# Performance work log

Hardware: AMD Instinct MI355X
Metric: run time of the kernel (lower is better)

Reference implementation:

```python
import jax, jax.numpy as jnp
import numpy as np

N, DIN, DOUT = 8192, 512, 256


def setup_inputs() -> dict:
    key = jax.random.key(0)
    ks = jax.random.split(key, 8)
    s_in = 1.0 / np.sqrt(DIN)   # ~ torch Linear default init scale
    s_out = 1.0 / np.sqrt(DOUT)
    return {
        "x": jax.random.normal(ks[0], (N, DIN), jnp.float32),
        "Wm": jax.random.normal(ks[1], (DIN, DOUT), jnp.float32) * s_in,
        "Wn": jax.random.normal(ks[2], (DIN, DOUT), jnp.float32) * s_in,
        "Wr": jax.random.normal(ks[3], (DIN, DOUT), jnp.float32) * s_in,
        "Wt": jax.random.normal(ks[4], (DIN, DOUT), jnp.float32) * s_in,
        "Wrg": jax.random.normal(ks[5], (DOUT, DOUT), jnp.float32) * s_out,
        "brg": jnp.zeros((DOUT,), jnp.float32),
        "Wlg": jax.random.normal(ks[6], (DOUT, DOUT), jnp.float32) * s_out,
        "blg": jnp.zeros((DOUT,), jnp.float32),
        "Wp": jax.random.normal(ks[7], (DOUT, 1), jnp.float32) * s_out,
        "bp": jnp.zeros((1,), jnp.float32),
    }


def reference(x, Wm, Wn, Wr, Wt, Wrg, brg, Wlg, blg, Wp, bp):
    n = x.shape[0]
    xm = x @ Wm                      # [N, 256]
    xn = x @ Wn                      # [N, 256]
    # pairwise Euclidean distance via GEMM trick (avoids O(N^2*D) diff tensor)
    sq = (jnp.sum(xm * xm, axis=-1)[:, None]
          + jnp.sum(xn * xn, axis=-1)[None, :]
          - 2.0 * (xm @ xn.T))       # [N, N]
    dist = jnp.sqrt(jnp.maximum(sq, 0.0)) * 0.5
    exps = jnp.exp(-dist) / (n / 64.0)
    eye = jnp.eye(n, dtype=x.dtype)
    adj = exps * (1.0 - eye) + eye   # unit diagonal, scaled off-diagonal
    xr = adj @ (x @ Wr)              # graph conv: [N,N]@[N,256]
    xl = x @ Wt
    w = jax.nn.sigmoid(xr @ Wrg + brg + xl @ Wlg + blg)
    feat = (1.0 - w) * xr + w * xl   # gated fusion
    score = feat @ Wp + bp           # [N, 1]
    return adj, score
```

## Files before the change

### kernel.cpp

```cpp
#include <hip/hip_runtime.h>
#include <stdint.h>

typedef __attribute__((ext_vector_type(8))) short bf16x8;
typedef __attribute__((ext_vector_type(4))) float f32x4;

__device__ __forceinline__ unsigned short f2bf(float f){
  unsigned u = __float_as_uint(f);
  u += 0x7FFFu + ((u >> 16) & 1u);
  return (unsigned short)(u >> 16);
}
__device__ __forceinline__ float bf2f(unsigned short s){
  return __uint_as_float(((unsigned)s) << 16);
}

__device__ __forceinline__ int lds_off(int r, int b){
  return r * 128 + (b ^ ((r & 7) << 4));
}

__device__ __forceinline__ void cp16(const unsigned short* g, unsigned short* l){
  __builtin_amdgcn_global_load_lds(
      (const __attribute__((address_space(1))) unsigned int*)g,
      (__attribute__((address_space(3))) unsigned int*)l, 16, 0, 0);
}

template<int ROWS, int NT>
__device__ __forceinline__ void stage_async(unsigned short* lds, const unsigned short* g,
                                            long row0, long stride, long k0, int tid){
#pragma unroll
  for (int c = tid; c < ROWS * 8; c += NT){
    int r = c >> 3, s = c & 7;
    int ss = s ^ (r & 7);
    cp16(g + (row0 + r) * stride + k0 + ss * 8, lds + (long)(c & ~63) * 8);
  }
}

template<int NT>
__device__ __forceinline__ void stage_adj(unsigned short* lds, const float* adj,
                                          long row0, long j, int tid){
#pragma unroll
  for (int u = 0; u < 1024 / NT; ++u){
    int c = tid + u * NT;
    int rr = c >> 3, s = c & 7;
    const f32x4* src = (const f32x4*)(adj + (row0 + rr) * 8192 + j + s * 8);
    f32x4 v0 = __builtin_nontemporal_load(src);
    f32x4 v1 = __builtin_nontemporal_load(src + 1);
    unsigned short tb[8] = { f2bf(v0[0]), f2bf(v0[1]), f2bf(v0[2]), f2bf(v0[3]),
                             f2bf(v1[0]), f2bf(v1[1]), f2bf(v1[2]), f2bf(v1[3]) };
    *(uint4*)((char*)lds + lds_off(rr, s * 16)) = *(const uint4*)tb;
  }
}

__device__ __forceinline__ int xcd_swz(int bid, int nwg){
  int q = nwg >> 3;
  return (bid & 7) * q + (bid >> 3);
}

__global__ __launch_bounds__(256) void k_prep(const float* x, const float* Wm, const float* Wn,
    const float* Wr, const float* Wt, const float* Wrg, const float* Wlg, const float* bp,
    unsigned short* WT, unsigned short* WcatT, unsigned short* xbf, float* nm, float* nn,
    float* score){
  long id = (long)blockIdx.x * 256 + threadIdx.x;
  if (id < 1024L * 512){
    int n = (int)(id >> 9), k = (int)(id & 511);
    const float* W = (n < 256) ? Wm : ((n < 512) ? Wn : ((n < 768) ? Wr : Wt));
    WT[id] = f2bf(W[(long)k * 256 + (n & 255)]);
  }
  if (id < 256L * 512){
    int n = (int)(id >> 9), k = (int)(id & 511);
    WcatT[id] = f2bf(k < 256 ? Wrg[(long)k * 256 + n] : Wlg[(long)(k - 256) * 256 + n]);
  }
  if (id < 8192){ score[id] = bp[0]; nm[id] = 0.f; nn[id] = 0.f; }
  long xe = id * 8;
  float4 v0 = *(const float4*)(x + xe);
  float4 v1 = *(const float4*)(x + xe + 4);
  unsigned short t[8] = { f2bf(v0.x), f2bf(v0.y), f2bf(v0.z), f2bf(v0.w),
                          f2bf(v1.x), f2bf(v1.y), f2bf(v1.z), f2bf(v1.w) };
  *(uint4*)(xbf + xe) = *(const uint4*)t;
}

__global__ __launch_bounds__(256, 3) void k_gemmA(const unsigned short* xbf, const unsigned short* WT,
    unsigned short* xm, unsigned short* xn, unsigned short* xwrT, unsigned short* xl,
    float* nm, float* nn){
  __shared__ unsigned short ldsA[128 * 64];
  __shared__ unsigned short ldsB[128 * 64];
  int tid = threadIdx.x, lane = tid & 63, w = tid >> 6;
  int r = lane & 15, gq = lane >> 4;
  int wi = w >> 1, wc = w & 1;
  int swz = xcd_swz(blockIdx.x, 512);
  int bm = swz & 63, bn = swz >> 6;

  f32x4 acc[4][4];
  f32x4 zero = {0.f, 0.f, 0.f, 0.f};
#pragma unroll
  for (int m = 0; m < 4; ++m)
#pragma unroll
    for (int n = 0; n < 4; ++n) acc[m][n] = zero;

  for (int k0 = 0; k0 < 512; k0 += 64){
    __syncthreads();
    stage_async<128, 256>(ldsA, xbf, (long)bm * 128, 512, k0, tid);
    stage_async<128, 256>(ldsB, WT, (long)bn * 128, 512, k0, tid);
    __syncthreads();
#pragma unroll
    for (int ks = 0; ks < 2; ++ks){
      int bb = ks * 64 + gq * 16;
      bf16x8 a[4], b[4];
#pragma unroll
      for (int m = 0; m < 4; ++m)
        a[m] = *(const bf16x8*)((const char*)ldsA + lds_off(wi * 64 + m * 16 + r, bb));
#pragma unroll
      for (int n = 0; n < 4; ++n)
        b[n] = *(const bf16x8*)((const char*)ldsB + lds_off(wc * 64 + n * 16 + r, bb));
#pragma unroll
      for (int m = 0; m < 4; ++m)
#pragma unroll
        for (int n = 0; n < 4; ++n)
          acc[m][n] = __builtin_amdgcn_mfma_f32_16x16x32_bf16(b[n], a[m], acc[m][n], 0, 0, 0);
    }
  }
#pragma unroll
  for (int m = 0; m < 4; ++m){
    int i = bm * 128 + wi * 64 + m * 16 + r;
#pragma unroll
    for (int n = 0; n < 4; ++n){
      int ng = bn * 128 + wc * 64 + n * 16 + gq * 4;
      int sector = ng >> 8, nc = ng & 255;
      unsigned short p[4] = { f2bf(acc[m][n][0]), f2bf(acc[m][n][1]),
                              f2bf(acc[m][n][2]), f2bf(acc[m][n][3]) };
      if (sector == 2){
#pragma unroll
        for (int q = 0; q < 4; ++q) xwrT[(long)(nc + q) * 8192 + i] = p[q];
      } else {
        unsigned short* dst = sector == 0 ? xm : (sector == 1 ? xn : xl);
        *(uint2*)(dst + (long)i * 256 + nc) = *(const uint2*)p;
      }
    }
    if (bn < 4){
      float s = 0.f;
#pragma unroll
      for (int n = 0; n < 4; ++n)
#pragma unroll
        for (int q = 0; q < 4; ++q) s += acc[m][n][q] * acc[m][n][q];
      s += __shfl_xor(s, 16);
      s += __shfl_xor(s, 32);
      if (gq == 0) atomicAdd(((bn < 2) ? nm : nn) + i, s);
    }
  }
}

__global__ __launch_bounds__(256, 2) void k_adj(const unsigned short* xm, const unsigned short* xn,
    const float* nm, const float* nn, float* adj){
  __shared__ char smem[65536];
  f32x4* ldsOut = (f32x4*)smem;

  int tid = threadIdx.x, lane = tid & 63, w = tid >> 6;
  int r = lane & 15, gq = lane >> 4;
  int wi = w >> 1, wj = w & 1;
  int swz = xcd_swz(blockIdx.x, 4096);
  int bm = swz & 63, bn = swz >> 6;

  f32x4 acc1[4][4];
  f32x4 zero = {0.f, 0.f, 0.f, 0.f};
#pragma unroll
  for (int m = 0; m < 4; ++m)
#pragma unroll
    for (int n = 0; n < 4; ++n) acc1[m][n] = zero;

  stage_async<128, 256>((unsigned short*)smem, xm, (long)bm * 128, 256, 0, tid);
  stage_async<128, 256>((unsigned short*)(smem + 16384), xn, (long)bn * 128, 256, 0, tid);
  __syncthreads();

#pragma unroll
  for (int t = 0; t < 4; ++t){
    char* cbuf = smem + (t & 1) * 32768;
    if (t < 3){
      char* nbuf = smem + ((t + 1) & 1) * 32768;
      stage_async<128, 256>((unsigned short*)nbuf, xm, (long)bm * 128, 256, (t + 1) * 64, tid);
      stage_async<128, 256>((unsigned short*)(nbuf + 16384), xn, (long)bn * 128, 256, (t + 1) * 64, tid);
    }
    unsigned short* ldsA = (unsigned short*)cbuf;
    unsigned short* ldsB = (unsigned short*)(cbuf + 16384);
    __builtin_amdgcn_s_setprio(1);
#pragma unroll
    for (int ks = 0; ks < 2; ++ks){
      int bb = ks * 64 + gq * 16;
      bf16x8 a[4], b[4];
#pragma unroll
      for (int m = 0; m < 4; ++m)
        a[m] = *(const bf16x8*)((const char*)ldsA + lds_off(wi * 64 + m * 16 + r, bb));
#pragma unroll
      for (int n = 0; n < 4; ++n)
        b[n] = *(const bf16x8*)((const char*)ldsB + lds_off(wj * 64 + n * 16 + r, bb));
#pragma unroll
      for (int m = 0; m < 4; ++m)
#pragma unroll
        for (int n = 0; n < 4; ++n)
          acc1[m][n] = __builtin_amdgcn_mfma_f32_16x16x32_bf16(b[n], a[m], acc1[m][n], 0, 0, 0);
    }
    __builtin_amdgcn_s_setprio(0);
    __syncthreads();
  }

  float nmi[4];
#pragma unroll
  for (int m = 0; m < 4; ++m) nmi[m] = nm[bm * 128 + wi * 64 + m * 16 + r];
#pragma unroll
  for (int n = 0; n < 4; ++n){
    int jb = bn * 128 + wj * 64 + n * 16 + gq * 4;
    float4 nn4 = *(const float4*)(nn + jb);
    const float nnq[4] = { nn4.x, nn4.y, nn4.z, nn4.w };
#pragma unroll
    for (int m = 0; m < 4; ++m){
      int i = bm * 128 + wi * 64 + m * 16 + r;
#pragma unroll
      for (int q = 0; q < 4; ++q){
        float sq = nmi[m] + nnq[q] - 2.f * acc1[m][n][q];
        float d = sqrtf(fmaxf(sq, 0.f)) * 0.5f;
        acc1[m][n][q] = (i == jb + q) ? 1.f : __expf(-d) * (1.f / 128.f);
      }
    }
  }

#pragma unroll
  for (int p = 0; p < 2; ++p){
    __syncthreads();
    if (wi == p){
#pragma unroll
      for (int m = 0; m < 4; ++m){
        int row64 = m * 16 + r;
#pragma unroll
        for (int n = 0; n < 4; ++n){
          int slot = wj * 16 + n * 4 + gq;
          ldsOut[row64 * 32 + (slot ^ (row64 & 7))] = acc1[m][n];
        }
      }
    }
    __syncthreads();
#pragma unroll
    for (int c = 0; c < 8; ++c){
      int rr = w * 16 + ((lane >> 3) << 1) + (c & 1);
      int slot = (c >> 1) * 8 + (lane & 7);
      f32x4 v = ldsOut[rr * 32 + (slot ^ (rr & 7))];
      long grow = (long)(bm * 128 + p * 64 + rr) * 8192 + bn * 128 + slot * 4;
      __builtin_nontemporal_store(v, (f32x4*)(adj + grow));
    }
  }
}

__global__ __launch_bounds__(512, 1) void k_xr(const float* adj,
    const unsigned short* xwrT, float* partial, int klen, int nblk){
  __shared__ char smem[98304];
  int tid = threadIdx.x, lane = tid & 63, w = tid >> 6;
  int r = lane & 15, gq = lane >> 4;
  int wi = w >> 2, wc = w & 3;
  int swz = xcd_swz(blockIdx.x, nblk);
  int bm = swz & 63, sp = swz >> 6;
  long j0 = (long)sp * klen;
  int nt = klen >> 6;

  f32x4 acc[4][4];
  f32x4 zero = {0.f, 0.f, 0.f, 0.f};
#pragma unroll
  for (int m = 0; m < 4; ++m)
#pragma unroll
    for (int n = 0; n < 4; ++n) acc[m][n] = zero;

  stage_adj<512>((unsigned short*)smem, adj, (long)bm * 128, j0, tid);
  stage_async<256, 512>((unsigned short*)(smem + 16384), xwrT, 0, 8192, j0, tid);
  __syncthreads();

  for (int t = 0; t < nt; ++t){
    char* cbuf = smem + (t & 1) * 49152;
    char* nbuf = smem + ((t & 1) ^ 1) * 49152;
    bool pf = (t + 1 < nt);
    long jn = j0 + (long)(t + 1) * 64;
    f32x4 av0[2], av1[2];
    int rra[2], ssa[2];
    if (pf){
#pragma unroll
      for (int u = 0; u < 2; ++u){
        int c = tid + u * 512;
        rra[u] = c >> 3; ssa[u] = c & 7;
        const f32x4* src = (const f32x4*)(adj + (long)(bm * 128 + rra[u]) * 8192 + jn + ssa[u] * 8);
        av0[u] = __builtin_nontemporal_load(src);
        av1[u] = __builtin_nontemporal_load(src + 1);
      }
      stage_async<256, 512>((unsigned short*)(nbuf + 16384), xwrT, 0, 8192, jn, tid);
    }
    unsigned short* ldsA = (unsigned short*)cbuf;
    unsigned short* ldsB = (unsigned short*)(cbuf + 16384);
    __builtin_amdgcn_s_setprio(1);
#pragma unroll
    for (int ks = 0; ks < 2; ++ks){
      int bb = ks * 64 + gq * 16;
      bf16x8 a[4], b[4];
#pragma unroll
      for (int m = 0; m < 4; ++m)
        a[m] = *(const bf16x8*)((const char*)ldsA + lds_off(wi * 64 + m * 16 + r, bb));
#pragma unroll
      for (int n = 0; n < 4; ++n)
        b[n] = *(const bf16x8*)((const char*)ldsB + lds_off(wc * 64 + n * 16 + r, bb));
#pragma unroll
      for (int m = 0; m < 4; ++m)
#pragma unroll
        for (int n = 0; n < 4; ++n)
          acc[m][n] = __builtin_amdgcn_mfma_f32_16x16x32_bf16(b[n], a[m], acc[m][n], 0, 0, 0);
    }
    __builtin_amdgcn_s_setprio(0);
    if (pf){
#pragma unroll
      for (int u = 0; u < 2; ++u){
        unsigned short tb[8] = { f2bf(av0[u][0]), f2bf(av0[u][1]), f2bf(av0[u][2]), f2bf(av0[u][3]),
                                 f2bf(av1[u][0]), f2bf(av1[u][1]), f2bf(av1[u][2]), f2bf(av1[u][3]) };
        *(uint4*)(nbuf + lds_off(rra[u], ssa[u] * 16)) = *(const uint4*)tb;
      }
    }
    __syncthreads();
  }

  float* dst = partial + (long)sp * 8192 * 256;
#pragma unroll
  for (int m = 0; m < 4; ++m){
    int i = bm * 128 + wi * 64 + m * 16 + r;
#pragma unroll
    for (int n = 0; n < 4; ++n){
      int cb = wc * 64 + n * 16 + gq * 4;
      __builtin_nontemporal_store(acc[m][n], (f32x4*)(dst + (long)i * 256 + cb));
    }
  }
}

__global__ __launch_bounds__(256) void k_reduce_xr(const float* partial, unsigned short* xr, int S){
  long idx = ((long)blockIdx.x * 256 + threadIdx.x) * 4;
  f32x4 a = __builtin_nontemporal_load((const f32x4*)(partial + idx));
  for (int s = 1; s < S; ++s){
    f32x4 b = __builtin_nontemporal_load((const f32x4*)(partial + (long)s * 8192 * 256 + idx));
    a += b;
  }
  unsigned short p[4] = { f2bf(a[0]), f2bf(a[1]), f2bf(a[2]), f2bf(a[3]) };
  *(uint2*)(xr + idx) = make_uint2((unsigned)p[0] | ((unsigned)p[1] << 16),
                                   (unsigned)p[2] | ((unsigned)p[3] << 16));
}

__global__ __launch_bounds__(512, 2) void k_gate(const unsigned short* xr, const unsigned short* xl,
    const unsigned short* WcatT, const float* brg, const float* blg,
    const float* Wp, float* score){
  __shared__ unsigned short ldsA[128 * 64];
  __shared__ unsigned short ldsB[256 * 64];
  int tid = threadIdx.x, lane = tid & 63, w = tid >> 6;
  int r = lane & 15, gq = lane >> 4;
  int wi = w >> 2, wc = w & 3;
  int bm = blockIdx.x;

  f32x4 acc[4][4];
  f32x4 zero = {0.f, 0.f, 0.f, 0.f};
#pragma unroll
  for (int m = 0; m < 4; ++m)
#pragma unroll
    for (int n = 0; n < 4; ++n) acc[m][n] = zero;

  for (int k0 = 0; k0 < 512; k0 += 64){
    const unsigned short* A = (k0 < 256) ? xr : xl;
    __syncthreads();
    stage_async<128, 512>(ldsA, A, (long)bm * 128, 256, k0 & 255, tid);
    stage_async<256, 512>(ldsB, WcatT, 0, 512, k0, tid);
    __syncthreads();
#pragma unroll
    for (int ks = 0; ks < 2; ++ks){
      int bb = ks * 64 + gq * 16;
      bf16x8 a[4], b[4];
#pragma unroll
      for (int m = 0; m < 4; ++m)
        a[m] = *(const bf16x8*)((const char*)ldsA + lds_off(wi * 64 + m * 16 + r, bb));
#pragma unroll
      for (int n = 0; n < 4; ++n)
        b[n] = *(const bf16x8*)((const char*)ldsB + lds_off(wc * 64 + n * 16 + r, bb));
#pragma unroll
      for (int m = 0; m < 4; ++m)
#pragma unroll
        for (int n = 0; n < 4; ++n)
          acc[m][n] = __builtin_amdgcn_mfma_f32_16x16x32_bf16(b[n], a[m], acc[m][n], 0, 0, 0);
    }
  }
#pragma unroll
  for (int m = 0; m < 4; ++m){
    int i = bm * 128 + wi * 64 + m * 16 + r;
    float part = 0.f;
#pragma unroll
    for (int n = 0; n < 4; ++n){
      int cb = wc * 64 + n * 16 + gq * 4;
      float4 b4  = *(const float4*)(brg + cb);
      float4 l4  = *(const float4*)(blg + cb);
      float4 wp4 = *(const float4*)(Wp + cb);
      unsigned short xr4[4], xl4[4];
      *(uint2*)xr4 = *(const uint2*)(xr + (long)i * 256 + cb);
      *(uint2*)xl4 = *(const uint2*)(xl + (long)i * 256 + cb);
      const float bq[4] = { b4.x, b4.y, b4.z, b4.w };
      const float lq[4] = { l4.x, l4.y, l4.z, l4.w };
      const float pq[4] = { wp4.x, wp4.y, wp4.z, wp4.w };
#pragma unroll
      for (int q = 0; q < 4; ++q){
        float arg = acc[m][n][q] + bq[q] + lq[q];
        float wv = 1.f / (1.f + __expf(-arg));
        float feat = (1.f - wv) * bf2f(xr4[q]) + wv * bf2f(xl4[q]);
        part += feat * pq[q];
      }
    }
    part += __shfl_xor(part, 16);
    part += __shfl_xor(part, 32);
    if (gq == 0) atomicAdd(score + i, part);
  }
}

extern "C" void kernel_launch(void* const* d_in, const int* in_sizes, int n_in,
                              void* d_out, int out_size, void* d_ws, size_t ws_size,
                              hipStream_t stream){
  const float* x   = (const float*)d_in[0];
  const float* Wm  = (const float*)d_in[1];
  const float* Wn  = (const float*)d_in[2];
  const float* Wr  = (const float*)d_in[3];
  const float* Wt  = (const float*)d_in[4];
  const float* Wrg = (const float*)d_in[5];
  const float* brg = (const float*)d_in[6];
  const float* Wlg = (const float*)d_in[7];
  const float* blg = (const float*)d_in[8];
  const float* Wp  = (const float*)d_in[9];
  const float* bp  = (const float*)d_in[10];

  float* adj   = (float*)d_out;
  float* score = adj + 8192L * 8192;

  char* wsb = (char*)d_ws;
  unsigned short* xm    = (unsigned short*)(wsb);
  unsigned short* xn    = (unsigned short*)(wsb + (4L  << 20));
  unsigned short* xwrT  = (unsigned short*)(wsb + (8L  << 20));
  unsigned short* xl    = (unsigned short*)(wsb + (12L << 20));
  unsigned short* xr    = (unsigned short*)(wsb + (16L << 20));
  float*          nm    = (float*)         (wsb + (20L << 20));
  float*          nn    = nm + 8192;
  unsigned short* WT    = (unsigned short*)(wsb + (21L << 20));
  unsigned short* WcatT = (unsigned short*)(wsb + (22L << 20));
  unsigned short* xbf   = (unsigned short*)(wsb + (23L << 20));
  float*          partial = (float*)(wsb + (31L << 20));

  int NS = 1;
  size_t base = 31L << 20;
  if      (ws_size >= base + 4 * (8L << 20)) NS = 4;
  else if (ws_size >= base + 2 * (8L << 20)) NS = 2;

  k_prep  <<<2048, 256, 0, stream>>>(x, Wm, Wn, Wr, Wt, Wrg, Wlg, bp, WT, WcatT, xbf, nm, nn, score);
  k_gemmA <<<512, 256, 0, stream>>>(xbf, WT, xm, xn, xwrT, xl, nm, nn);
  k_adj   <<<4096, 256, 0, stream>>>(xm, xn, nm, nn, adj);
  k_xr    <<<64 * NS, 512, 0, stream>>>(adj, xwrT, partial, 8192 / NS, 64 * NS);
  k_reduce_xr<<<2048, 256, 0, stream>>>(partial, xr, NS);
  k_gate  <<<64, 512, 0, stream>>>(xr, xl, WcatT, brg, blg, Wp, score);
}
```

Before: 261.6 us.

## Emit bf16 adjacency copy for graph-conv GEMM and fuse partial reduction into gate

k_adj now rounds the adjacency to bf16, stages it through LDS, and writes both a bf16 copy to workspace and the fp32 output, which is now expanded from the rounded bf16 values. k_xr streams the bf16 copy with async global-to-LDS loads instead of loading fp32 rows and converting them in registers, which halves its read volume and simplifies its prefetch. The separate k_reduce_xr kernel is removed: k_gate sums the split-K partials itself and keeps the xr/xl fragments it needs in registers. In exchange, k_adj writes an extra 128 MB, the fp32 adj output loses precision to bf16 rounding, and the partial buffer moves to a much higher workspace offset.

```diff
diff --git a/kernel.cpp b/kernel.cpp
--- a/kernel.cpp
+++ b/kernel.cpp
@@ -3,6 +3,7 @@
 
 typedef __attribute__((ext_vector_type(8))) short bf16x8;
 typedef __attribute__((ext_vector_type(4))) float f32x4;
+typedef __attribute__((ext_vector_type(4))) unsigned int u32x4;
 
 __device__ __forceinline__ unsigned short f2bf(float f){
   unsigned u = __float_as_uint(f);
@@ -16,6 +17,9 @@
 __device__ __forceinline__ int lds_off(int r, int b){
   return r * 128 + (b ^ ((r & 7) << 4));
 }
+__device__ __forceinline__ int ldsP_off(int r, int b){
+  return r * 256 + (b ^ ((r & 7) << 4));
+}
 
 __device__ __forceinline__ void cp16(const unsigned short* g, unsigned short* l){
   __builtin_amdgcn_global_load_lds(
@@ -31,22 +35,6 @@
     int r = c >> 3, s = c & 7;
     int ss = s ^ (r & 7);
     cp16(g + (row0 + r) * stride + k0 + ss * 8, lds + (long)(c & ~63) * 8);
-  }
-}
-
-template<int NT>
-__device__ __forceinline__ void stage_adj(unsigned short* lds, const float* adj,
-                                          long row0, long j, int tid){
-#pragma unroll
-  for (int u = 0; u < 1024 / NT; ++u){
-    int c = tid + u * NT;
-    int rr = c >> 3, s = c & 7;
-    const f32x4* src = (const f32x4*)(adj + (row0 + rr) * 8192 + j + s * 8);
-    f32x4 v0 = __builtin_nontemporal_load(src);
-    f32x4 v1 = __builtin_nontemporal_load(src + 1);
-    unsigned short tb[8] = { f2bf(v0[0]), f2bf(v0[1]), f2bf(v0[2]), f2bf(v0[3]),
-                             f2bf(v1[0]), f2bf(v1[1]), f2bf(v1[2]), f2bf(v1[3]) };
-    *(uint4*)((char*)lds + lds_off(rr, s * 16)) = *(const uint4*)tb;
   }
 }
 
@@ -149,9 +137,9 @@
 }
 
 __global__ __launch_bounds__(256, 2) void k_adj(const unsigned short* xm, const unsigned short* xn,
-    const float* nm, const float* nn, float* adj){
+    const float* nm, const float* nn, float* adj, unsigned short* adjbf){
   __shared__ char smem[65536];
-  f32x4* ldsOut = (f32x4*)smem;
+  char* ldsP = smem;
 
   int tid = threadIdx.x, lane = tid & 63, w = tid >> 6;
   int r = lane & 15, gq = lane >> 4;
@@ -206,55 +194,50 @@
   for (int m = 0; m < 4; ++m) nmi[m] = nm[bm * 128 + wi * 64 + m * 16 + r];
 #pragma unroll
   for (int n = 0; n < 4; ++n){
-    int jb = bn * 128 + wj * 64 + n * 16 + gq * 4;
+    int jl0 = wj * 64 + n * 16 + gq * 4;
+    int jb = bn * 128 + jl0;
     float4 nn4 = *(const float4*)(nn + jb);
     const float nnq[4] = { nn4.x, nn4.y, nn4.z, nn4.w };
 #pragma unroll
     for (int m = 0; m < 4; ++m){
-      int i = bm * 128 + wi * 64 + m * 16 + r;
+      int il = wi * 64 + m * 16 + r;
+      int i = bm * 128 + il;
+      unsigned short pv[4];
 #pragma unroll
       for (int q = 0; q < 4; ++q){
         float sq = nmi[m] + nnq[q] - 2.f * acc1[m][n][q];
         float d = sqrtf(fmaxf(sq, 0.f)) * 0.5f;
-        acc1[m][n][q] = (i == jb + q) ? 1.f : __expf(-d) * (1.f / 128.f);
+        float v = (i == jb + q) ? 1.f : __expf(-d) * (1.f / 128.f);
+        pv[q] = f2bf(v);
       }
-    }
-  }
-
-#pragma unroll
-  for (int p = 0; p < 2; ++p){
-    __syncthreads();
-    if (wi == p){
-#pragma unroll
-      for (int m = 0; m < 4; ++m){
-        int row64 = m * 16 + r;
-#pragma unroll
-        for (int n = 0; n < 4; ++n){
-          int slot = wj * 16 + n * 4 + gq;
-          ldsOut[row64 * 32 + (slot ^ (row64 & 7))] = acc1[m][n];
-        }
-      }
-    }
-    __syncthreads();
-#pragma unroll
-    for (int c = 0; c < 8; ++c){
-      int rr = w * 16 + ((lane >> 3) << 1) + (c & 1);
-      int slot = (c >> 1) * 8 + (lane & 7);
-      f32x4 v = ldsOut[rr * 32 + (slot ^ (rr & 7))];
-      long grow = (long)(bm * 128 + p * 64 + rr) * 8192 + bn * 128 + slot * 4;
-      __builtin_nontemporal_store(v, (f32x4*)(adj + grow));
-    }
-  }
-}
-
-__global__ __launch_bounds__(512, 1) void k_xr(const float* adj,
-    const unsigned short* xwrT, float* partial, int klen, int nblk){
+      *(uint2*)(ldsP + ldsP_off(il, jl0 * 2)) = *(const uint2*)pv;
+    }
+  }
+  __syncthreads();
+
+#pragma unroll
+  for (int o = 0; o < 8; ++o){
+    int c = o * 256 + tid;
+    int row = c >> 4, cs = c & 15;
+    unsigned short pb[8];
+    *(uint4*)pb = *(const uint4*)(ldsP + ldsP_off(row, cs * 16));
+    long ge = (long)(bm * 128 + row) * 8192 + bn * 128 + cs * 8;
+    __builtin_nontemporal_store(*(const u32x4*)pb, (u32x4*)(adjbf + ge));
+    f32x4 v0 = { bf2f(pb[0]), bf2f(pb[1]), bf2f(pb[2]), bf2f(pb[3]) };
+    f32x4 v1 = { bf2f(pb[4]), bf2f(pb[5]), bf2f(pb[6]), bf2f(pb[7]) };
+    __builtin_nontemporal_store(v0, (f32x4*)(adj + ge));
+    __builtin_nontemporal_store(v1, (f32x4*)(adj + ge + 4));
+  }
+}
+
+__global__ __launch_bounds__(512, 1) void k_xr(const unsigned short* adjbf,
+    const unsigned short* xwrT, float* partial, int klen, int NS){
   __shared__ char smem[98304];
   int tid = threadIdx.x, lane = tid & 63, w = tid >> 6;
   int r = lane & 15, gq = lane >> 4;
   int wi = w >> 2, wc = w & 3;
-  int swz = xcd_swz(blockIdx.x, nblk);
-  int bm = swz & 63, sp = swz >> 6;
+  int sp = blockIdx.x % NS;
+  int bm = blockIdx.x / NS;
   long j0 = (long)sp * klen;
   int nt = klen >> 6;
 
@@ -265,26 +248,16 @@
 #pragma unroll
     for (int n = 0; n < 4; ++n) acc[m][n] = zero;
 
-  stage_adj<512>((unsigned short*)smem, adj, (long)bm * 128, j0, tid);
+  stage_async<128, 512>((unsigned short*)smem, adjbf, (long)bm * 128, 8192, j0, tid);
   stage_async<256, 512>((unsigned short*)(smem + 16384), xwrT, 0, 8192, j0, tid);
   __syncthreads();
 
   for (int t = 0; t < nt; ++t){
     char* cbuf = smem + (t & 1) * 49152;
-    char* nbuf = smem + ((t & 1) ^ 1) * 49152;
-    bool pf = (t + 1 < nt);
-    long jn = j0 + (long)(t + 1) * 64;
-    f32x4 av0[2], av1[2];
-    int rra[2], ssa[2];
-    if (pf){
-#pragma unroll
-      for (int u = 0; u < 2; ++u){
-        int c = tid + u * 512;
-        rra[u] = c >> 3; ssa[u] = c & 7;
-        const f32x4* src = (const f32x4*)(adj + (long)(bm * 128 + rra[u]) * 8192 + jn + ssa[u] * 8);
-        av0[u] = __builtin_nontemporal_load(src);
-        av1[u] = __builtin_nontemporal_load(src + 1);
-      }
+    if (t + 1 < nt){
+      char* nbuf = smem + ((t + 1) & 1) * 49152;
+      long jn = j0 + (long)(t + 1) * 64;
+      stage_async<128, 512>((unsigned short*)nbuf, adjbf, (long)bm * 128, 8192, jn, tid);
       stage_async<256, 512>((unsigned short*)(nbuf + 16384), xwrT, 0, 8192, jn, tid);
     }
     unsigned short* ldsA = (unsigned short*)cbuf;
@@ -307,14 +280,6 @@
           acc[m][n] = __builtin_amdgcn_mfma_f32_16x16x32_bf16(b[n], a[m], acc[m][n], 0, 0, 0);
     }
     __builtin_amdgcn_s_setprio(0);
-    if (pf){
-#pragma unroll
-      for (int u = 0; u < 2; ++u){
-        unsigned short tb[8] = { f2bf(av0[u][0]), f2bf(av0[u][1]), f2bf(av0[u][2]), f2bf(av0[u][3]),
-                                 f2bf(av1[u][0]), f2bf(av1[u][1]), f2bf(av1[u][2]), f2bf(av1[u][3]) };
-        *(uint4*)(nbuf + lds_off(rra[u], ssa[u] * 16)) = *(const uint4*)tb;
-      }
-    }
     __syncthreads();
   }
 
@@ -330,21 +295,9 @@
   }
 }
 
-__global__ __launch_bounds__(256) void k_reduce_xr(const float* partial, unsigned short* xr, int S){
-  long idx = ((long)blockIdx.x * 256 + threadIdx.x) * 4;
-  f32x4 a = __builtin_nontemporal_load((const f32x4*)(partial + idx));
-  for (int s = 1; s < S; ++s){
-    f32x4 b = __builtin_nontemporal_load((const f32x4*)(partial + (long)s * 8192 * 256 + idx));
-    a += b;
-  }
-  unsigned short p[4] = { f2bf(a[0]), f2bf(a[1]), f2bf(a[2]), f2bf(a[3]) };
-  *(uint2*)(xr + idx) = make_uint2((unsigned)p[0] | ((unsigned)p[1] << 16),
-                                   (unsigned)p[2] | ((unsigned)p[3] << 16));
-}
-
-__global__ __launch_bounds__(512, 2) void k_gate(const unsigned short* xr, const unsigned short* xl,
-    const unsigned short* WcatT, const float* brg, const float* blg,
-    const float* Wp, float* score){
+__global__ __launch_bounds__(512, 2) void k_gate(const float* partial, int S,
+    const unsigned short* xl, const unsigned short* WcatT,
+    const float* brg, const float* blg, const float* Wp, float* score){
   __shared__ unsigned short ldsA[128 * 64];
   __shared__ unsigned short ldsB[256 * 64];
   int tid = threadIdx.x, lane = tid & 63, w = tid >> 6;
@@ -359,12 +312,44 @@
 #pragma unroll
     for (int n = 0; n < 4; ++n) acc[m][n] = zero;
 
-  for (int k0 = 0; k0 < 512; k0 += 64){
-    const unsigned short* A = (k0 < 256) ? xr : xl;
-    __syncthreads();
-    stage_async<128, 512>(ldsA, A, (long)bm * 128, 256, k0 & 255, tid);
-    stage_async<256, 512>(ldsB, WcatT, 0, 512, k0, tid);
-    __syncthreads();
+  uint2 xrf[4][4], xlf[4][4];
+
+  for (int t = 0; t < 8; ++t){
+    __syncthreads();
+    if (t < 4){
+#pragma unroll
+      for (int u = 0; u < 2; ++u){
+        int c = tid + u * 512;
+        int rr = c >> 3, s = c & 7;
+        long gi = (long)(bm * 128 + rr) * 256 + t * 64 + s * 8;
+        f32x4 a0 = __builtin_nontemporal_load((const f32x4*)(partial + gi));
+        f32x4 a1 = __builtin_nontemporal_load((const f32x4*)(partial + gi + 4));
+        for (int sp = 1; sp < S; ++sp){
+          long go = (long)sp * 8192 * 256 + gi;
+          a0 += __builtin_nontemporal_load((const f32x4*)(partial + go));
+          a1 += __builtin_nontemporal_load((const f32x4*)(partial + go + 4));
+        }
+        unsigned short tb[8] = { f2bf(a0[0]), f2bf(a0[1]), f2bf(a0[2]), f2bf(a0[3]),
+                                 f2bf(a1[0]), f2bf(a1[1]), f2bf(a1[2]), f2bf(a1[3]) };
+        *(uint4*)((char*)ldsA + lds_off(rr, s * 16)) = *(const uint4*)tb;
+      }
+    } else {
+      stage_async<128, 512>(ldsA, xl, (long)bm * 128, 256, (t - 4) * 64, tid);
+    }
+    stage_async<256, 512>(ldsB, WcatT, 0, 512, (long)t * 64, tid);
+    __syncthreads();
+
+    if (t == wc || t == wc + 4){
+#pragma unroll
+      for (int m = 0; m < 4; ++m){
+        int il = wi * 64 + m * 16 + r;
+#pragma unroll
+        for (int n = 0; n < 4; ++n){
+          uint2 v = *(const uint2*)((const char*)ldsA + lds_off(il, (n * 16 + gq * 4) * 2));
+          if (t < 4) xrf[m][n] = v; else xlf[m][n] = v;
+        }
+      }
+    }
 #pragma unroll
     for (int ks = 0; ks < 2; ++ks){
       int bb = ks * 64 + gq * 16;
@@ -382,6 +367,7 @@
           acc[m][n] = __builtin_amdgcn_mfma_f32_16x16x32_bf16(b[n], a[m], acc[m][n], 0, 0, 0);
     }
   }
+
 #pragma unroll
   for (int m = 0; m < 4; ++m){
     int i = bm * 128 + wi * 64 + m * 16 + r;
@@ -392,9 +378,8 @@
       float4 b4  = *(const float4*)(brg + cb);
       float4 l4  = *(const float4*)(blg + cb);
       float4 wp4 = *(const float4*)(Wp + cb);
-      unsigned short xr4[4], xl4[4];
-      *(uint2*)xr4 = *(const uint2*)(xr + (long)i * 256 + cb);
-      *(uint2*)xl4 = *(const uint2*)(xl + (long)i * 256 + cb);
+      const unsigned short* xr4 = (const unsigned short*)&xrf[m][n];
+      const unsigned short* xl4 = (const unsigned short*)&xlf[m][n];
       const float bq[4] = { b4.x, b4.y, b4.z, b4.w };
       const float lq[4] = { l4.x, l4.y, l4.z, l4.w };
       const float pq[4] = { wp4.x, wp4.y, wp4.z, wp4.w };
@@ -435,23 +420,22 @@
   unsigned short* xn    = (unsigned short*)(wsb + (4L  << 20));
   unsigned short* xwrT  = (unsigned short*)(wsb + (8L  << 20));
   unsigned short* xl    = (unsigned short*)(wsb + (12L << 20));
-  unsigned short* xr    = (unsigned short*)(wsb + (16L << 20));
   float*          nm    = (float*)         (wsb + (20L << 20));
   float*          nn    = nm + 8192;
   unsigned short* WT    = (unsigned short*)(wsb + (21L << 20));
   unsigned short* WcatT = (unsigned short*)(wsb + (22L << 20));
   unsigned short* xbf   = (unsigned short*)(wsb + (23L << 20));
-  float*          partial = (float*)(wsb + (31L << 20));
-
+  unsigned short* adjbf = (unsigned short*)(wsb + (31L << 20));
+  float*          partial = (float*)(wsb + (159L << 20));
+
+  size_t base = 159L << 20;
   int NS = 1;
-  size_t base = 31L << 20;
   if      (ws_size >= base + 4 * (8L << 20)) NS = 4;
   else if (ws_size >= base + 2 * (8L << 20)) NS = 2;
 
   k_prep  <<<2048, 256, 0, stream>>>(x, Wm, Wn, Wr, Wt, Wrg, Wlg, bp, WT, WcatT, xbf, nm, nn, score);
   k_gemmA <<<512, 256, 0, stream>>>(xbf, WT, xm, xn, xwrT, xl, nm, nn);
-  k_adj   <<<4096, 256, 0, stream>>>(xm, xn, nm, nn, adj);
-  k_xr    <<<64 * NS, 512, 0, stream>>>(adj, xwrT, partial, 8192 / NS, 64 * NS);
-  k_reduce_xr<<<2048, 256, 0, stream>>>(partial, xr, NS);
-  k_gate  <<<64, 512, 0, stream>>>(xr, xl, WcatT, brg, blg, Wp, score);
-}
+  k_adj   <<<4096, 256, 0, stream>>>(xm, xn, nm, nn, adj, adjbf);
+  k_xr    <<<64 * NS, 512, 0, stream>>>(adjbf, xwrT, partial, 8192 / NS, NS);
+  k_gate  <<<64, 512, 0, stream>>>(partial, NS, xl, WcatT, brg, blg, Wp, score);
+}
```

Measured after the change: 294.7 us. 12.7% more time.

## Fuse split-K reduction into gate kernel, raise split count, use cached loads

Applied to the files above, without the earlier changes.

Removes the separate split-K reduce kernel: the gate kernel now sums the fp32 partials directly while staging its A tile, and keeps the xr/xl values it needs for the epilogue in registers instead of reloading them. The split count can rise to 8 when workspace allows, and the XCD block swizzle is replaced by a plain interleave that places the splits of one row block next to each other. Nontemporal loads and stores on adj and the partials become ordinary cached accesses, which may let adj stay in L2/MALL between the adj and xr kernels. The trade-off is that the 64-block gate kernel now reads more partial data, and more partial traffic is generated overall.

```diff
diff --git a/kernel.cpp b/kernel.cpp
--- a/kernel.cpp
+++ b/kernel.cpp
@@ -42,8 +42,8 @@
     int c = tid + u * NT;
     int rr = c >> 3, s = c & 7;
     const f32x4* src = (const f32x4*)(adj + (row0 + rr) * 8192 + j + s * 8);
-    f32x4 v0 = __builtin_nontemporal_load(src);
-    f32x4 v1 = __builtin_nontemporal_load(src + 1);
+    f32x4 v0 = src[0];
+    f32x4 v1 = src[1];
     unsigned short tb[8] = { f2bf(v0[0]), f2bf(v0[1]), f2bf(v0[2]), f2bf(v0[3]),
                              f2bf(v1[0]), f2bf(v1[1]), f2bf(v1[2]), f2bf(v1[3]) };
     *(uint4*)((char*)lds + lds_off(rr, s * 16)) = *(const uint4*)tb;
@@ -242,19 +242,19 @@
       int slot = (c >> 1) * 8 + (lane & 7);
       f32x4 v = ldsOut[rr * 32 + (slot ^ (rr & 7))];
       long grow = (long)(bm * 128 + p * 64 + rr) * 8192 + bn * 128 + slot * 4;
-      __builtin_nontemporal_store(v, (f32x4*)(adj + grow));
+      *(f32x4*)(adj + grow) = v;
     }
   }
 }
 
 __global__ __launch_bounds__(512, 1) void k_xr(const float* adj,
-    const unsigned short* xwrT, float* partial, int klen, int nblk){
+    const unsigned short* xwrT, float* partial, int klen, int NS){
   __shared__ char smem[98304];
   int tid = threadIdx.x, lane = tid & 63, w = tid >> 6;
   int r = lane & 15, gq = lane >> 4;
   int wi = w >> 2, wc = w & 3;
-  int swz = xcd_swz(blockIdx.x, nblk);
-  int bm = swz & 63, sp = swz >> 6;
+  int sp = blockIdx.x % NS;
+  int bm = blockIdx.x / NS;
   long j0 = (long)sp * klen;
   int nt = klen >> 6;
 
@@ -282,8 +282,8 @@
         int c = tid + u * 512;
         rra[u] = c >> 3; ssa[u] = c & 7;
         const f32x4* src = (const f32x4*)(adj + (long)(bm * 128 + rra[u]) * 8192 + jn + ssa[u] * 8);
-        av0[u] = __builtin_nontemporal_load(src);
-        av1[u] = __builtin_nontemporal_load(src + 1);
+        av0[u] = src[0];
+        av1[u] = src[1];
       }
       stage_async<256, 512>((unsigned short*)(nbuf + 16384), xwrT, 0, 8192, jn, tid);
     }
@@ -325,26 +325,14 @@
 #pragma unroll
     for (int n = 0; n < 4; ++n){
       int cb = wc * 64 + n * 16 + gq * 4;
-      __builtin_nontemporal_store(acc[m][n], (f32x4*)(dst + (long)i * 256 + cb));
-    }
-  }
-}
-
-__global__ __launch_bounds__(256) void k_reduce_xr(const float* partial, unsigned short* xr, int S){
-  long idx = ((long)blockIdx.x * 256 + threadIdx.x) * 4;
-  f32x4 a = __builtin_nontemporal_load((const f32x4*)(partial + idx));
-  for (int s = 1; s < S; ++s){
-    f32x4 b = __builtin_nontemporal_load((const f32x4*)(partial + (long)s * 8192 * 256 + idx));
-    a += b;
-  }
-  unsigned short p[4] = { f2bf(a[0]), f2bf(a[1]), f2bf(a[2]), f2bf(a[3]) };
-  *(uint2*)(xr + idx) = make_uint2((unsigned)p[0] | ((unsigned)p[1] << 16),
-                                   (unsigned)p[2] | ((unsigned)p[3] << 16));
-}
-
-__global__ __launch_bounds__(512, 2) void k_gate(const unsigned short* xr, const unsigned short* xl,
-    const unsigned short* WcatT, const float* brg, const float* blg,
-    const float* Wp, float* score){
+      *(f32x4*)(dst + (long)i * 256 + cb) = acc[m][n];
+    }
+  }
+}
+
+__global__ __launch_bounds__(512, 2) void k_gate(const float* partial, int S,
+    const unsigned short* xl, const unsigned short* WcatT,
+    const float* brg, const float* blg, const float* Wp, float* score){
   __shared__ unsigned short ldsA[128 * 64];
   __shared__ unsigned short ldsB[256 * 64];
   int tid = threadIdx.x, lane = tid & 63, w = tid >> 6;
@@ -359,12 +347,44 @@
 #pragma unroll
     for (int n = 0; n < 4; ++n) acc[m][n] = zero;
 
-  for (int k0 = 0; k0 < 512; k0 += 64){
-    const unsigned short* A = (k0 < 256) ? xr : xl;
-    __syncthreads();
-    stage_async<128, 512>(ldsA, A, (long)bm * 128, 256, k0 & 255, tid);
-    stage_async<256, 512>(ldsB, WcatT, 0, 512, k0, tid);
-    __syncthreads();
+  uint2 xrf[4][4], xlf[4][4];
+
+  for (int t = 0; t < 8; ++t){
+    __syncthreads();
+    if (t < 4){
+#pragma unroll
+      for (int u = 0; u < 2; ++u){
+        int c = tid + u * 512;
+        int rr = c >> 3, s = c & 7;
+        long gi = (long)(bm * 128 + rr) * 256 + t * 64 + s * 8;
+        f32x4 a0 = *(const f32x4*)(partial + gi);
+        f32x4 a1 = *(const f32x4*)(partial + gi + 4);
+        for (int sp = 1; sp < S; ++sp){
+          long go = (long)sp * 8192 * 256 + gi;
+          a0 += *(const f32x4*)(partial + go);
+          a1 += *(const f32x4*)(partial + go + 4);
+        }
+        unsigned short tb[8] = { f2bf(a0[0]), f2bf(a0[1]), f2bf(a0[2]), f2bf(a0[3]),
+                                 f2bf(a1[0]), f2bf(a1[1]), f2bf(a1[2]), f2bf(a1[3]) };
+        *(uint4*)((char*)ldsA + lds_off(rr, s * 16)) = *(const uint4*)tb;
+      }
+    } else {
+      stage_async<128, 512>(ldsA, xl, (long)bm * 128, 256, (t - 4) * 64, tid);
+    }
+    stage_async<256, 512>(ldsB, WcatT, 0, 512, (long)t * 64, tid);
+    __syncthreads();
+
+    if (t == wc || t == wc + 4){
+#pragma unroll
+      for (int m = 0; m < 4; ++m){
+        int il = wi * 64 + m * 16 + r;
+#pragma unroll
+        for (int n = 0; n < 4; ++n){
+          uint2 v = *(const uint2*)((const char*)ldsA + lds_off(il, (n * 16 + gq * 4) * 2));
+          if (t < 4) xrf[m][n] = v; else xlf[m][n] = v;
+        }
+      }
+    }
 #pragma unroll
     for (int ks = 0; ks < 2; ++ks){
       int bb = ks * 64 + gq * 16;
@@ -382,6 +402,7 @@
           acc[m][n] = __builtin_amdgcn_mfma_f32_16x16x32_bf16(b[n], a[m], acc[m][n], 0, 0, 0);
     }
   }
+
 #pragma unroll
   for (int m = 0; m < 4; ++m){
     int i = bm * 128 + wi * 64 + m * 16 + r;
@@ -392,9 +413,8 @@
       float4 b4  = *(const float4*)(brg + cb);
       float4 l4  = *(const float4*)(blg + cb);
       float4 wp4 = *(const float4*)(Wp + cb);
-      unsigned short xr4[4], xl4[4];
-      *(uint2*)xr4 = *(const uint2*)(xr + (long)i * 256 + cb);
-      *(uint2*)xl4 = *(const uint2*)(xl + (long)i * 256 + cb);
+      const unsigned short* xr4 = (const unsigned short*)&xrf[m][n];
+      const unsigned short* xl4 = (const unsigned short*)&xlf[m][n];
       const float bq[4] = { b4.x, b4.y, b4.z, b4.w };
       const float lq[4] = { l4.x, l4.y, l4.z, l4.w };
       const float pq[4] = { wp4.x, wp4.y, wp4.z, wp4.w };
@@ -435,7 +455,6 @@
   unsigned short* xn    = (unsigned short*)(wsb + (4L  << 20));
   unsigned short* xwrT  = (unsigned short*)(wsb + (8L  << 20));
   unsigned short* xl    = (unsigned short*)(wsb + (12L << 20));
-  unsigned short* xr    = (unsigned short*)(wsb + (16L << 20));
   float*          nm    = (float*)         (wsb + (20L << 20));
   float*          nn    = nm + 8192;
   unsigned short* WT    = (unsigned short*)(wsb + (21L << 20));
@@ -443,15 +462,15 @@
   unsigned short* xbf   = (unsigned short*)(wsb + (23L << 20));
   float*          partial = (float*)(wsb + (31L << 20));
 
+  size_t base = 31L << 20;
   int NS = 1;
-  size_t base = 31L << 20;
-  if      (ws_size >= base + 4 * (8L << 20)) NS = 4;
+  if      (ws_size >= base + 8 * (8L << 20)) NS = 8;
+  else if (ws_size >= base + 4 * (8L << 20)) NS = 4;
   else if (ws_size >= base + 2 * (8L << 20)) NS = 2;
 
   k_prep  <<<2048, 256, 0, stream>>>(x, Wm, Wn, Wr, Wt, Wrg, Wlg, bp, WT, WcatT, xbf, nm, nn, score);
   k_gemmA <<<512, 256, 0, stream>>>(xbf, WT, xm, xn, xwrT, xl, nm, nn);
   k_adj   <<<4096, 256, 0, stream>>>(xm, xn, nm, nn, adj);
-  k_xr    <<<64 * NS, 512, 0, stream>>>(adj, xwrT, partial, 8192 / NS, 64 * NS);
-  k_reduce_xr<<<2048, 256, 0, stream>>>(partial, xr, NS);
-  k_gate  <<<64, 512, 0, stream>>>(xr, xl, WcatT, brg, blg, Wp, score);
-}
+  k_xr    <<<64 * NS, 512, 0, stream>>>(adj, xwrT, partial, 8192 / NS, NS);
+  k_gate  <<<64, 512, 0, stream>>>(partial, NS, xl, WcatT, brg, blg, Wp, score);
+}
```

New measurement: 296.9 us. 1.13x slower.
